# Optimization experiments

Measured on AMD Instinct MI355X. Metric: run time of the kernel, lower is better.

The kernel has to match this reference:

```python
import jax, jax.numpy as jnp
import numpy as np

N0, N1, N2, DEG = 100000, 50000, 25000, 16
IN, HID, OUT = 256, 128, 128
H1, H2 = 2, 1
E1, E2 = N1 * DEG, N2 * DEG


def setup_inputs() -> dict:
    key = jax.random.key(0)
    ks = jax.random.split(key, 16)
    x = jax.random.normal(ks[0], (N0, IN), dtype=jnp.float32)
    # neighbor-sampled bipartite edges: each dst node has DEG sampled src neighbors
    row1 = jnp.repeat(jnp.arange(N1, dtype=jnp.int32), DEG)
    col1 = jax.random.randint(ks[1], (E1,), 0, N0, dtype=jnp.int32)
    t1 = jax.random.randint(ks[2], (E1,), 0, 100, dtype=jnp.int32)
    row2 = jnp.repeat(jnp.arange(N2, dtype=jnp.int32), DEG)
    col2 = jax.random.randint(ks[3], (E2,), 0, N1, dtype=jnp.int32)
    t2 = jax.random.randint(ks[4], (E2,), 0, 100, dtype=jnp.int32)
    s_in = 1.0 / np.sqrt(IN)
    s_h = 1.0 / np.sqrt(HID)
    s_bn = 1.0 / np.sqrt(HID * H1)
    return dict(
        x=x, row1=row1, col1=col1, t1=t1, row2=row2, col2=col2, t2=t2,
        time=10, interval=20,
        Ws1=jax.random.normal(ks[5], (IN, H1 * HID), jnp.float32) * s_in,
        Wd1=jax.random.normal(ks[6], (IN, H1 * HID), jnp.float32) * s_in,
        as1=jax.random.normal(ks[7], (H1, HID), jnp.float32) * s_h,
        ad1=jax.random.normal(ks[8], (H1, HID), jnp.float32) * s_h,
        b1=jnp.zeros((H1 * HID,), jnp.float32),
        g1=jnp.ones((H1 * HID,), jnp.float32),
        beta1=jnp.zeros((H1 * HID,), jnp.float32),
        m1=jnp.zeros((H1 * HID,), jnp.float32),
        v1=jnp.ones((H1 * HID,), jnp.float32),
        Ws2=jax.random.normal(ks[9], (H1 * HID, H2 * OUT), jnp.float32) * s_bn,
        Wd2=jax.random.normal(ks[10], (H1 * HID, H2 * OUT), jnp.float32) * s_bn,
        as2=jax.random.normal(ks[11], (H2, OUT), jnp.float32) * s_h,
        ad2=jax.random.normal(ks[12], (H2, OUT), jnp.float32) * s_h,
        b2=jnp.zeros((H2 * OUT,), jnp.float32),
    )


def gat_conv(hs, hd, row, col, mask, att_s, att_d, n_dst):
    # hs: [Ns,H,C] transformed src feats, hd: [Nd,H,C]; row=dst idx, col=src idx per edge
    a_s = jnp.sum(hs * att_s, axis=-1)  # [Ns,H]
    a_d = jnp.sum(hd * att_d, axis=-1)  # [Nd,H]
    e = jax.nn.leaky_relu(a_s[col] + a_d[row], negative_slope=0.2)  # [E,H]
    e = jnp.where(mask[:, None], e, -jnp.inf)
    m = jax.ops.segment_max(e, row, num_segments=n_dst)  # [Nd,H]
    m = jnp.where(jnp.isfinite(m), m, 0.0)
    ex = jnp.where(mask[:, None], jnp.exp(e - m[row]), 0.0)
    denom = jax.ops.segment_sum(ex, row, num_segments=n_dst)
    alpha = ex / jnp.maximum(denom[row], 1e-16)  # edge softmax over incoming edges
    out = jax.ops.segment_sum(alpha[:, :, None] * hs[col], row, num_segments=n_dst)
    return out  # [Nd,H,C]


def _forward(x, Ws1, Wd1, as1, ad1, b1, g1, beta1, m1, v1,
             Ws2, Wd2, as2, ad2, b2,
             row1, col1, t1, row2, col2, t2, time, interval):
    # temporal edge masking: keep edges with timestamp in [time, time+interval)
    mask1 = (t1 >= time) & (t1 < time + interval)
    mask2 = (t2 >= time) & (t2 < time + interval)
    # ---- layer 1: GATConv(IN -> HID, heads=H1, concat=True) ----
    hs = (x @ Ws1).reshape(N0, H1, HID)
    hd = (x[:N1] @ Wd1).reshape(N1, H1, HID)
    h = gat_conv(hs, hd, row1, col1, mask1, as1, ad1, N1).reshape(N1, H1 * HID) + b1
    # BatchNorm1d (eval: running stats), then leaky_relu (slope 0.01); dropout off (eval)
    h = (h - m1) * jax.lax.rsqrt(v1 + 1e-5) * g1 + beta1
    h = jax.nn.leaky_relu(h, negative_slope=0.01)
    # ---- layer 2: GATConv(H1*HID -> OUT, heads=H2, concat=False) ----
    hs2 = (h @ Ws2).reshape(N1, H2, OUT)
    hd2 = (h[:N2] @ Wd2).reshape(N2, H2, OUT)
    out = gat_conv(hs2, hd2, row2, col2, mask2, as2, ad2, N2)
    out = jnp.mean(out, axis=1) + b2  # concat=False -> mean over heads
    return out  # [N2, OUT]


def reference(x, row1, col1, t1, row2, col2, t2, time, interval,
              Ws1, Wd1, as1, ad1, b1, g1, beta1, m1, v1,
              Ws2, Wd2, as2, ad2, b2):
    return _forward(x, Ws1, Wd1, as1, ad1, b1, g1, beta1, m1, v1,
                    Ws2, Wd2, as2, ad2, b2,
                    row1, col1, t1, row2, col2, t2, time, interval)
```

## Files before the change

kernel.cpp:

```cpp
#include <hip/hip_runtime.h>
#include <hip/hip_bf16.h>

#define N0C 100000
#define N1C 50000
#define N2C 25000

typedef _Float16 f16;
typedef _Float16 f16x2 __attribute__((ext_vector_type(2)));
typedef _Float16 f16x4 __attribute__((ext_vector_type(4)));
typedef _Float16 f16x8 __attribute__((ext_vector_type(8)));
typedef float f32x16 __attribute__((ext_vector_type(16)));

typedef const __attribute__((address_space(1))) unsigned int guint;
typedef __attribute__((address_space(3))) unsigned int luint;
__device__ __forceinline__ void gload16(const void* g, void* l) {
    __builtin_amdgcn_global_load_lds((guint*)g, (luint*)l, 16, 0, 0);
}

__device__ __forceinline__ f16x8 cvt8(float4 a, float4 b) {
    return (f16x8){(f16)a.x, (f16)a.y, (f16)a.z, (f16)a.w,
                   (f16)b.x, (f16)b.y, (f16)b.z, (f16)b.w};
}

__global__ void prep1_kernel(const float* __restrict__ Ws1, const float* __restrict__ Wd1,
                             const float* __restrict__ as1, const float* __restrict__ ad1,
                             const float* __restrict__ Ws2, const float* __restrict__ Wd2,
                             const float* __restrict__ as2, const float* __restrict__ ad2,
                             const float* __restrict__ b1, const float* __restrict__ g1,
                             const float* __restrict__ beta1, const float* __restrict__ m1,
                             const float* __restrict__ v1,
                             float* __restrict__ e1, float* __restrict__ e2,
                             float* __restrict__ bns, float* __restrict__ bnt) {
    int k = blockIdx.x, lane = threadIdx.x;
    float s0 = 0, s1 = 0, d0 = 0, d1 = 0, t0 = 0, t1 = 0;
    for (int c = lane; c < 128; c += 64) {
        s0 += Ws1[k * 256 + c] * as1[c];
        s1 += Ws1[k * 256 + 128 + c] * as1[128 + c];
        d0 += Wd1[k * 256 + c] * ad1[c];
        d1 += Wd1[k * 256 + 128 + c] * ad1[128 + c];
        t0 += Ws2[k * 128 + c] * as2[c];
        t1 += Wd2[k * 128 + c] * ad2[c];
    }
    for (int d = 1; d < 64; d <<= 1) {
        s0 += __shfl_xor(s0, d); s1 += __shfl_xor(s1, d);
        d0 += __shfl_xor(d0, d); d1 += __shfl_xor(d1, d);
        t0 += __shfl_xor(t0, d); t1 += __shfl_xor(t1, d);
    }
    if (lane == 0) {
        e1[k * 4 + 0] = s0; e1[k * 4 + 1] = s1; e1[k * 4 + 2] = d0; e1[k * 4 + 3] = d1;
        e2[k * 2 + 0] = t0; e2[k * 2 + 1] = t1;
        float sc = g1[k] * rsqrtf(v1[k] + 1e-5f);
        bns[k] = sc;
        bnt[k] = (b1[k] - m1[k]) * sc + beta1[k];
    }
}

__global__ void prep2_kernel(const float* __restrict__ Ws1, const float* __restrict__ Ws2,
                             const float* __restrict__ e1, const float* __restrict__ e2,
                             f16* __restrict__ bfl1, f16* __restrict__ bfl2) {
    int i = blockIdx.x * 256 + threadIdx.x;
    if (i < 73728) {
        int j = i & 7, lane = (i >> 3) & 63, kb = (i >> 9) & 15, nt = i >> 13;
        int c = lane & 31, hi = lane >> 5;
        int k = kb * 16 + hi * 8 + j;
        float v;
        if (nt < 8) v = Ws1[k * 256 + nt * 32 + c];
        else v = (c < 4) ? e1[k * 4 + c] : 0.f;
        bfl1[i] = (f16)v;
    } else {
        int i2 = i - 73728;
        if (i2 < 40960) {
            int j = i2 & 7, lane = (i2 >> 3) & 63, kb = (i2 >> 9) & 15, nt = i2 >> 13;
            int c = lane & 31, hi = lane >> 5;
            int k = kb * 16 + hi * 8 + j;
            float v;
            if (nt < 4) v = Ws2[k * 128 + nt * 32 + c];
            else v = (c < 2) ? e2[k * 2 + c] : 0.f;
            bfl2[i2] = (f16)v;
        }
    }
}

__global__ __launch_bounds__(512, 4) void gemm1_kernel(
    const float* __restrict__ x, const f16* __restrict__ bfl,
    f16* __restrict__ hs, float* __restrict__ as_out, float* __restrict__ ad_out) {
    __shared__ __align__(16) unsigned char smA[2][8192];
    __shared__ __align__(16) unsigned char smB[2][18432];
    const int t = threadIdx.x;
    const int wave = t >> 6, lane = t & 63;
    const int wr = wave & 3, wg = wave >> 2;
    const int col = lane & 31, hi = lane >> 5;
    const int r0 = blockIdx.x * 128;

    const int arow = t >> 2, aq = t & 3;
    const int grow_a = r0 + arow;
    const bool aval = grow_a < N0C;
    const float4* abase = (const float4*)(x + (size_t)grow_a * 256);
    const int aslot = (((arow >> 5) * 2 + (aq >> 1)) * 64 + (aq & 1) * 32 + (arow & 31)) * 16;

    float4 a0, a1;
    if (aval) { a0 = abase[aq * 2]; a1 = abase[aq * 2 + 1]; }
    else { a0 = make_float4(0.f, 0.f, 0.f, 0.f); a1 = a0; }
    for (int c = wave; c < 18; c += 8) {
        int nt = c >> 1, kbl = c & 1;
        gload16(bfl + ((size_t)(nt * 16 + kbl) * 64 + lane) * 8, smB[0] + c * 1024 + lane * 16);
    }
    *(f16x8*)(smA[0] + aslot) = cvt8(a0, a1);
    __syncthreads();

    f32x16 acc[5] = {};
    for (int ch = 0; ch < 8; ch++) {
        const int cur = ch & 1, nxt = cur ^ 1;
        const bool pre = ch < 7;
        if (pre) {
            if (aval) {
                const float4* p = abase + (ch + 1) * 8 + aq * 2;
                a0 = p[0]; a1 = p[1];
            }
            for (int c = wave; c < 18; c += 8) {
                int nt = c >> 1, kbl = c & 1;
                gload16(bfl + ((size_t)(nt * 16 + (ch + 1) * 2 + kbl) * 64 + lane) * 8,
                        smB[nxt] + c * 1024 + lane * 16);
            }
        }
#pragma unroll
        for (int kb = 0; kb < 2; kb++) {
            f16x8 af = *(const f16x8*)(smA[cur] + ((wr * 2 + kb) * 64 + lane) * 16);
            if (wg == 0) {
#pragma unroll
                for (int j = 0; j < 5; j++) {
                    f16x8 bf = *(const f16x8*)(smB[cur] + (j * 2 + kb) * 1024 + lane * 16);
                    acc[j] = __builtin_amdgcn_mfma_f32_32x32x16_f16(af, bf, acc[j], 0, 0, 0);
                }
            } else {
#pragma unroll
                for (int j = 0; j < 4; j++) {
                    f16x8 bf = *(const f16x8*)(smB[cur] + ((5 + j) * 2 + kb) * 1024 + lane * 16);
                    acc[j] = __builtin_amdgcn_mfma_f32_32x32x16_f16(af, bf, acc[j], 0, 0, 0);
                }
            }
        }
        if (pre) *(f16x8*)(smA[nxt] + aslot) = cvt8(a0, a1);
        __syncthreads();
    }

    const int rbase = r0 + wr * 32 + 4 * hi;
    if (wg == 0) {
#pragma unroll
        for (int j = 0; j < 5; j++)
#pragma unroll
            for (int r = 0; r < 16; r++) {
                int grow = rbase + (r & 3) + 8 * (r >> 2);
                if (grow < N0C) hs[(size_t)grow * 256 + j * 32 + col] = (f16)acc[j][r];
            }
    } else {
#pragma unroll
        for (int j = 0; j < 3; j++)
#pragma unroll
            for (int r = 0; r < 16; r++) {
                int grow = rbase + (r & 3) + 8 * (r >> 2);
                if (grow < N0C) hs[(size_t)grow * 256 + (5 + j) * 32 + col] = (f16)acc[j][r];
            }
#pragma unroll
        for (int r = 0; r < 16; r++) {
            int grow = rbase + (r & 3) + 8 * (r >> 2);
            float v = acc[3][r];
            if (col < 2) {
                if (grow < N0C) as_out[grow * 2 + col] = v;
            } else if (col < 4) {
                if (grow < N1C) ad_out[grow * 2 + (col - 2)] = v;
            }
        }
    }
}

__global__ __launch_bounds__(512, 4) void gemm2_kernel(
    const f16* __restrict__ h, const f16* __restrict__ bfl,
    f16* __restrict__ hs2, float* __restrict__ as_out, float* __restrict__ ad_out) {
    __shared__ __align__(16) unsigned char smA[2][8192];
    __shared__ __align__(16) unsigned char smB[2][10240];
    const int t = threadIdx.x;
    const int wave = t >> 6, lane = t & 63;
    const int wr = wave & 3, wg = wave >> 2;
    const int col = lane & 31, hi = lane >> 5;
    const int r0 = blockIdx.x * 128;

    const int wrA = wave >> 1, kbA = wave & 1;
    int arowg = r0 + wrA * 32 + col;
    if (arowg > N1C - 1) arowg = N1C - 1;
    const f16* asrc = h + (size_t)arowg * 256 + kbA * 16 + hi * 8;

    gload16(asrc, smA[0] + wave * 1024 + lane * 16);
    for (int c = wave; c < 10; c += 8) {
        int nt = c >> 1, kbl = c & 1;
        gload16(bfl + ((size_t)(nt * 16 + kbl) * 64 + lane) * 8, smB[0] + c * 1024 + lane * 16);
    }
    __syncthreads();

    f32x16 acc[3] = {};
    for (int ch = 0; ch < 8; ch++) {
        const int cur = ch & 1, nxt = cur ^ 1;
        const bool pre = ch < 7;
        if (pre) {
            gload16(asrc + (ch + 1) * 32, smA[nxt] + wave * 1024 + lane * 16);
            for (int c = wave; c < 10; c += 8) {
                int nt = c >> 1, kbl = c & 1;
                gload16(bfl + ((size_t)(nt * 16 + (ch + 1) * 2 + kbl) * 64 + lane) * 8,
                        smB[nxt] + c * 1024 + lane * 16);
            }
        }
#pragma unroll
        for (int kb = 0; kb < 2; kb++) {
            f16x8 af = *(const f16x8*)(smA[cur] + ((wr * 2 + kb) * 64 + lane) * 16);
            if (wg == 0) {
#pragma unroll
                for (int j = 0; j < 3; j++) {
                    f16x8 bf = *(const f16x8*)(smB[cur] + (j * 2 + kb) * 1024 + lane * 16);
                    acc[j] = __builtin_amdgcn_mfma_f32_32x32x16_f16(af, bf, acc[j], 0, 0, 0);
                }
            } else {
#pragma unroll
                for (int j = 0; j < 2; j++) {
                    f16x8 bf = *(const f16x8*)(smB[cur] + ((3 + j) * 2 + kb) * 1024 + lane * 16);
                    acc[j] = __builtin_amdgcn_mfma_f32_32x32x16_f16(af, bf, acc[j], 0, 0, 0);
                }
            }
        }
        __syncthreads();
    }

    const int rbase = r0 + wr * 32 + 4 * hi;
    if (wg == 0) {
#pragma unroll
        for (int j = 0; j < 3; j++)
#pragma unroll
            for (int r = 0; r < 16; r++) {
                int grow = rbase + (r & 3) + 8 * (r >> 2);
                if (grow < N1C) hs2[(size_t)grow * 128 + j * 32 + col] = (f16)acc[j][r];
            }
    } else {
#pragma unroll
        for (int r = 0; r < 16; r++) {
            int grow = rbase + (r & 3) + 8 * (r >> 2);
            if (grow < N1C) hs2[(size_t)grow * 128 + 3 * 32 + col] = (f16)acc[0][r];
        }
#pragma unroll
        for (int r = 0; r < 16; r++) {
            int grow = rbase + (r & 3) + 8 * (r >> 2);
            float v = acc[1][r];
            if (col == 0) {
                if (grow < N1C) as_out[grow] = v;
            } else if (col == 1) {
                if (grow < N2C) ad_out[grow] = v;
            }
        }
    }
}

__global__ void agg1_kernel(const int* __restrict__ col1, const int* __restrict__ t1,
                            const int* __restrict__ timep, const int* __restrict__ intervalp,
                            const float* __restrict__ a_s, const float* __restrict__ a_d,
                            const f16* __restrict__ hs,
                            const float* __restrict__ bns, const float* __restrict__ bnt,
                            f16* __restrict__ h) {
    int wid = (blockIdx.x * blockDim.x + threadIdx.x) >> 6;
    if (wid >= N1C) return;
    int lane = threadIdx.x & 63;
    int T = timep[0], I = intervalp[0];
    int j = lane & 15;
    int c = col1[wid * 16 + j];
    int tv = t1[wid * 16 + j];
    bool mk = (tv >= T) && (tv < T + I);
    float e0 = -INFINITY, e1 = -INFINITY;
    if (mk) {
        float s0 = a_s[c * 2 + 0] + a_d[wid * 2 + 0];
        float s1 = a_s[c * 2 + 1] + a_d[wid * 2 + 1];
        e0 = s0 > 0.f ? s0 : 0.2f * s0;
        e1 = s1 > 0.f ? s1 : 0.2f * s1;
    }
    float m0 = e0, m1 = e1;
#pragma unroll
    for (int d = 1; d < 16; d <<= 1) {
        m0 = fmaxf(m0, __shfl_xor(m0, d));
        m1 = fmaxf(m1, __shfl_xor(m1, d));
    }
    float ex0 = mk ? __expf(e0 - m0) : 0.f;
    float ex1 = mk ? __expf(e1 - m1) : 0.f;
    float s0 = ex0, s1 = ex1;
#pragma unroll
    for (int d = 1; d < 16; d <<= 1) {
        s0 += __shfl_xor(s0, d);
        s1 += __shfl_xor(s1, d);
    }
    float r0 = 1.f / fmaxf(s0, 1e-16f);
    float r1 = 1.f / fmaxf(s1, 1e-16f);
    unsigned long long mb = __ballot(mk) & 0xFFFFull;
    int head = lane >> 5;
    float rden = head ? r1 : r0;
    float acc0 = 0.f, acc1 = 0.f, acc2 = 0.f, acc3 = 0.f;
    while (mb) {
        int jj = __builtin_ctzll(mb);
        mb &= mb - 1;
        int cj = __shfl(c, jj);
        float w0 = __shfl(ex0, jj), w1 = __shfl(ex1, jj);
        float w = (head ? w1 : w0) * rden;
        f16x4 v = *(const f16x4*)(hs + (size_t)cj * 256 + lane * 4);
        acc0 += w * (float)v[0];
        acc1 += w * (float)v[1];
        acc2 += w * (float)v[2];
        acc3 += w * (float)v[3];
    }
    int cb = lane * 4;
    float4 sc = *(const float4*)(bns + cb);
    float4 sh = *(const float4*)(bnt + cb);
    float o0 = acc0 * sc.x + sh.x; o0 = o0 > 0.f ? o0 : 0.01f * o0;
    float o1 = acc1 * sc.y + sh.y; o1 = o1 > 0.f ? o1 : 0.01f * o1;
    float o2 = acc2 * sc.z + sh.z; o2 = o2 > 0.f ? o2 : 0.01f * o2;
    float o3 = acc3 * sc.w + sh.w; o3 = o3 > 0.f ? o3 : 0.01f * o3;
    f16x4 ov = {(f16)o0, (f16)o1, (f16)o2, (f16)o3};
    *(f16x4*)(h + (size_t)wid * 256 + cb) = ov;
}

__global__ void agg2_kernel(const int* __restrict__ col2, const int* __restrict__ t2,
                            const int* __restrict__ timep, const int* __restrict__ intervalp,
                            const float* __restrict__ a_s, const float* __restrict__ a_d,
                            const f16* __restrict__ hs2,
                            const float* __restrict__ b2, float* __restrict__ out) {
    int wid = (blockIdx.x * blockDim.x + threadIdx.x) >> 6;
    if (wid >= N2C) return;
    int lane = threadIdx.x & 63;
    int T = timep[0], I = intervalp[0];
    int j = lane & 15;
    int c = col2[wid * 16 + j];
    int tv = t2[wid * 16 + j];
    bool mk = (tv >= T) && (tv < T + I);
    float e = -INFINITY;
    if (mk) {
        float s = a_s[c] + a_d[wid];
        e = s > 0.f ? s : 0.2f * s;
    }
    float m = e;
#pragma unroll
    for (int d = 1; d < 16; d <<= 1) m = fmaxf(m, __shfl_xor(m, d));
    float ex = mk ? __expf(e - m) : 0.f;
    float s = ex;
#pragma unroll
    for (int d = 1; d < 16; d <<= 1) s += __shfl_xor(s, d);
    float r = 1.f / fmaxf(s, 1e-16f);
    unsigned long long mb = __ballot(mk) & 0xFFFFull;
    float acc0 = 0.f, acc1 = 0.f;
    while (mb) {
        int jj = __builtin_ctzll(mb);
        mb &= mb - 1;
        int cj = __shfl(c, jj);
        float w = __shfl(ex, jj) * r;
        f16x2 v = *(const f16x2*)(hs2 + (size_t)cj * 128 + lane * 2);
        acc0 += w * (float)v[0];
        acc1 += w * (float)v[1];
    }
    float2 o = make_float2(acc0 + b2[lane * 2], acc1 + b2[lane * 2 + 1]);
    *(float2*)(out + (size_t)wid * 128 + lane * 2) = o;
}

extern "C" void kernel_launch(void* const* d_in, const int* in_sizes, int n_in,
                              void* d_out, int out_size, void* d_ws, size_t ws_size,
                              hipStream_t stream) {
    const float* x = (const float*)d_in[0];
    const int* col1 = (const int*)d_in[2];
    const int* t1 = (const int*)d_in[3];
    const int* col2 = (const int*)d_in[5];
    const int* t2 = (const int*)d_in[6];
    const int* timep = (const int*)d_in[7];
    const int* intervalp = (const int*)d_in[8];
    const float* Ws1 = (const float*)d_in[9];
    const float* Wd1 = (const float*)d_in[10];
    const float* as1 = (const float*)d_in[11];
    const float* ad1 = (const float*)d_in[12];
    const float* b1 = (const float*)d_in[13];
    const float* g1 = (const float*)d_in[14];
    const float* beta1 = (const float*)d_in[15];
    const float* m1 = (const float*)d_in[16];
    const float* v1 = (const float*)d_in[17];
    const float* Ws2 = (const float*)d_in[18];
    const float* Wd2 = (const float*)d_in[19];
    const float* as2 = (const float*)d_in[20];
    const float* ad2 = (const float*)d_in[21];
    const float* b2 = (const float*)d_in[22];
    float* out = (float*)d_out;

    char* ws = (char*)d_ws;
    size_t off = 0;
    auto alloc = [&](size_t bytes) {
        size_t o = off;
        off += (bytes + 511) & ~(size_t)511;
        return o;
    };
    f16* hs = (f16*)(ws + alloc((size_t)N0C * 256 * 2));
    f16* h = (f16*)(ws + alloc((size_t)N1C * 256 * 2));
    f16* hs2 = (f16*)(ws + alloc((size_t)N1C * 128 * 2));
    float* a_s1 = (float*)(ws + alloc((size_t)N0C * 2 * 4));
    float* a_d1 = (float*)(ws + alloc((size_t)N1C * 2 * 4));
    float* a_s2 = (float*)(ws + alloc((size_t)N1C * 4));
    float* a_d2 = (float*)(ws + alloc((size_t)N2C * 4));
    f16* bfl1 = (f16*)(ws + alloc((size_t)73728 * 2));
    f16* bfl2 = (f16*)(ws + alloc((size_t)40960 * 2));
    float* e1 = (float*)(ws + alloc(1024 * 4));
    float* e2 = (float*)(ws + alloc(512 * 4));
    float* bns = (float*)(ws + alloc(256 * 4));
    float* bnt = (float*)(ws + alloc(256 * 4));

    prep1_kernel<<<256, 64, 0, stream>>>(Ws1, Wd1, as1, ad1, Ws2, Wd2, as2, ad2,
                                         b1, g1, beta1, m1, v1, e1, e2, bns, bnt);
    prep2_kernel<<<448, 256, 0, stream>>>(Ws1, Ws2, e1, e2, bfl1, bfl2);
    gemm1_kernel<<<(N0C + 127) / 128, 512, 0, stream>>>(x, bfl1, hs, a_s1, a_d1);
    agg1_kernel<<<N1C / 4, 256, 0, stream>>>(col1, t1, timep, intervalp,
                                             a_s1, a_d1, hs, bns, bnt, h);
    gemm2_kernel<<<(N1C + 127) / 128, 512, 0, stream>>>(h, bfl2, hs2, a_s2, a_d2);
    agg2_kernel<<<N2C / 4, 256, 0, stream>>>(col2, t2, timep, intervalp,
                                             a_s2, a_d2, hs2, b2, out);
}
```

Baseline: 103.7 us.

## Restructure layer-1 GEMM into 32-row tiles with split-K waves and swizzled LDS

The layer-1 projection GEMM now uses a 2D grid of 32-row tiles. Each 640-thread block loads the whole 32x256 fp32 A tile once into XOR-swizzled LDS as fp16, then gives each pair of waves one 32-column output tile with the K dimension split in half. B fragments are read straight from global memory instead of being double-buffered through LDS, and the two K halves are combined through LDS before storing. The aim is much higher parallelism and occupancy with less pipeline synchronisation, at the cost of reading the x rows twice (once per grid column) and losing row-bounds checks, which holds only because N0 is a multiple of 32.

```diff
diff --git a/kernel.cpp b/kernel.cpp
--- a/kernel.cpp
+++ b/kernel.cpp
@@ -15,11 +15,6 @@
 typedef __attribute__((address_space(3))) unsigned int luint;
 __device__ __forceinline__ void gload16(const void* g, void* l) {
     __builtin_amdgcn_global_load_lds((guint*)g, (luint*)l, 16, 0, 0);
-}
-
-__device__ __forceinline__ f16x8 cvt8(float4 a, float4 b) {
-    return (f16x8){(f16)a.x, (f16)a.y, (f16)a.z, (f16)a.w,
-                   (f16)b.x, (f16)b.y, (f16)b.z, (f16)b.w};
 }
 
 __global__ void prep1_kernel(const float* __restrict__ Ws1, const float* __restrict__ Wd1,
@@ -81,94 +76,73 @@
     }
 }
 
-__global__ __launch_bounds__(512, 4) void gemm1_kernel(
+__global__ __launch_bounds__(640, 8) void gemm1_kernel(
     const float* __restrict__ x, const f16* __restrict__ bfl,
     f16* __restrict__ hs, float* __restrict__ as_out, float* __restrict__ ad_out) {
-    __shared__ __align__(16) unsigned char smA[2][8192];
-    __shared__ __align__(16) unsigned char smB[2][18432];
+    __shared__ __align__(16) unsigned char smA[20480];
     const int t = threadIdx.x;
     const int wave = t >> 6, lane = t & 63;
-    const int wr = wave & 3, wg = wave >> 2;
+    const int ntl = wave >> 1, kh = wave & 1;
+    const int nt0 = blockIdx.x * 5 + ntl;
+    const int nt = nt0 > 8 ? 8 : nt0;
     const int col = lane & 31, hi = lane >> 5;
-    const int r0 = blockIdx.x * 128;
-
-    const int arow = t >> 2, aq = t & 3;
-    const int grow_a = r0 + arow;
-    const bool aval = grow_a < N0C;
-    const float4* abase = (const float4*)(x + (size_t)grow_a * 256);
-    const int aslot = (((arow >> 5) * 2 + (aq >> 1)) * 64 + (aq & 1) * 32 + (arow & 31)) * 16;
-
-    float4 a0, a1;
-    if (aval) { a0 = abase[aq * 2]; a1 = abase[aq * 2 + 1]; }
-    else { a0 = make_float4(0.f, 0.f, 0.f, 0.f); a1 = a0; }
-    for (int c = wave; c < 18; c += 8) {
-        int nt = c >> 1, kbl = c & 1;
-        gload16(bfl + ((size_t)(nt * 16 + kbl) * 64 + lane) * 8, smB[0] + c * 1024 + lane * 16);
-    }
-    *(f16x8*)(smA[0] + aslot) = cvt8(a0, a1);
+    const int r0 = blockIdx.y * 32;
+
+    if (t < 512) {
+        int r = t >> 4, s = t & 15;
+        const float4* src = (const float4*)(x + (size_t)(r0 + r) * 256) + s;
+#pragma unroll
+        for (int p = 0; p < 4; p++) {
+            float4 v = src[16 * p];
+            int q = s + 16 * p;
+            int kb = q >> 2, hp = (q >> 1) & 1, hf = q & 1;
+            f16x4 h4 = {(f16)v.x, (f16)v.y, (f16)v.z, (f16)v.w};
+            int byt = (((kb * 64 + hp * 32 + r) * 16) ^ ((kb & 7) << 4)) + hf * 8;
+            *(f16x4*)(smA + byt) = h4;
+        }
+    }
     __syncthreads();
 
-    f32x16 acc[5] = {};
-    for (int ch = 0; ch < 8; ch++) {
-        const int cur = ch & 1, nxt = cur ^ 1;
-        const bool pre = ch < 7;
-        if (pre) {
-            if (aval) {
-                const float4* p = abase + (ch + 1) * 8 + aq * 2;
-                a0 = p[0]; a1 = p[1];
-            }
-            for (int c = wave; c < 18; c += 8) {
-                int nt = c >> 1, kbl = c & 1;
-                gload16(bfl + ((size_t)(nt * 16 + (ch + 1) * 2 + kbl) * 64 + lane) * 8,
-                        smB[nxt] + c * 1024 + lane * 16);
-            }
-        }
-#pragma unroll
-        for (int kb = 0; kb < 2; kb++) {
-            f16x8 af = *(const f16x8*)(smA[cur] + ((wr * 2 + kb) * 64 + lane) * 16);
-            if (wg == 0) {
-#pragma unroll
-                for (int j = 0; j < 5; j++) {
-                    f16x8 bf = *(const f16x8*)(smB[cur] + (j * 2 + kb) * 1024 + lane * 16);
-                    acc[j] = __builtin_amdgcn_mfma_f32_32x32x16_f16(af, bf, acc[j], 0, 0, 0);
+    f32x16 acc = {};
+#pragma unroll
+    for (int g = 0; g < 2; g++) {
+        f16x8 b[4];
+#pragma unroll
+        for (int i = 0; i < 4; i++)
+            b[i] = *(const f16x8*)(bfl + ((size_t)(nt * 16 + kh * 8 + g * 4 + i) * 64 + lane) * 8);
+#pragma unroll
+        for (int i = 0; i < 4; i++) {
+            int kb = kh * 8 + g * 4 + i;
+            f16x8 af = *(const f16x8*)(smA + (((kb * 64 + hi * 32 + col) * 16) ^ ((kb & 7) << 4)));
+            acc = __builtin_amdgcn_mfma_f32_32x32x16_f16(af, b[i], acc, 0, 0, 0);
+        }
+    }
+    __syncthreads();
+
+    float* rb = (float*)smA;
+    if (kh == 1) {
+#pragma unroll
+        for (int r = 0; r < 16; r++) rb[(r * 5 + ntl) * 64 + lane] = acc[r];
+    }
+    __syncthreads();
+    if (kh == 0 && nt0 <= 8) {
+        if (nt0 < 8) {
+#pragma unroll
+            for (int r = 0; r < 16; r++) {
+                int grow = r0 + (r & 3) + 8 * (r >> 2) + 4 * hi;
+                hs[(size_t)grow * 256 + nt0 * 32 + col] =
+                    (f16)(acc[r] + rb[(r * 5 + ntl) * 64 + lane]);
+            }
+        } else {
+#pragma unroll
+            for (int r = 0; r < 16; r++) {
+                int grow = r0 + (r & 3) + 8 * (r >> 2) + 4 * hi;
+                float v = acc[r] + rb[(r * 5 + ntl) * 64 + lane];
+                if (col < 2) {
+                    as_out[grow * 2 + col] = v;
+                } else if (col < 4) {
+                    if (grow < N1C) ad_out[grow * 2 + (col - 2)] = v;
                 }
-            } else {
-#pragma unroll
-                for (int j = 0; j < 4; j++) {
-                    f16x8 bf = *(const f16x8*)(smB[cur] + ((5 + j) * 2 + kb) * 1024 + lane * 16);
-                    acc[j] = __builtin_amdgcn_mfma_f32_32x32x16_f16(af, bf, acc[j], 0, 0, 0);
-                }
-            }
-        }
-        if (pre) *(f16x8*)(smA[nxt] + aslot) = cvt8(a0, a1);
-        __syncthreads();
-    }
-
-    const int rbase = r0 + wr * 32 + 4 * hi;
-    if (wg == 0) {
-#pragma unroll
-        for (int j = 0; j < 5; j++)
-#pragma unroll
-            for (int r = 0; r < 16; r++) {
-                int grow = rbase + (r & 3) + 8 * (r >> 2);
-                if (grow < N0C) hs[(size_t)grow * 256 + j * 32 + col] = (f16)acc[j][r];
-            }
-    } else {
-#pragma unroll
-        for (int j = 0; j < 3; j++)
-#pragma unroll
-            for (int r = 0; r < 16; r++) {
-                int grow = rbase + (r & 3) + 8 * (r >> 2);
-                if (grow < N0C) hs[(size_t)grow * 256 + (5 + j) * 32 + col] = (f16)acc[j][r];
-            }
-#pragma unroll
-        for (int r = 0; r < 16; r++) {
-            int grow = rbase + (r & 3) + 8 * (r >> 2);
-            float v = acc[3][r];
-            if (col < 2) {
-                if (grow < N0C) as_out[grow * 2 + col] = v;
-            } else if (col < 4) {
-                if (grow < N1C) ad_out[grow * 2 + (col - 2)] = v;
             }
         }
     }
@@ -412,7 +386,7 @@
     prep1_kernel<<<256, 64, 0, stream>>>(Ws1, Wd1, as1, ad1, Ws2, Wd2, as2, ad2,
                                          b1, g1, beta1, m1, v1, e1, e2, bns, bnt);
     prep2_kernel<<<448, 256, 0, stream>>>(Ws1, Ws2, e1, e2, bfl1, bfl2);
-    gemm1_kernel<<<(N0C + 127) / 128, 512, 0, stream>>>(x, bfl1, hs, a_s1, a_d1);
+    gemm1_kernel<<<dim3(2, 3125), 640, 0, stream>>>(x, bfl1, hs, a_s1, a_d1);
     agg1_kernel<<<N1C / 4, 256, 0, stream>>>(col1, t1, timep, intervalp,
                                              a_s1, a_d1, hs, bns, bnt, h);
     gemm2_kernel<<<(N1C + 127) / 128, 512, 0, stream>>>(h, bfl2, hs2, a_s2, a_d2);
```

Measured after the change: 112.1 us. 1.08x slower.

## Stream fp32 A tiles directly into LDS via async loads with XOR swizzle

Applied to the files above, without the earlier changes.

The GEMM1 A operand (x in fp32) is now fetched with global_load_lds directly into a doubled-size LDS buffer using an XOR-swizzled layout, instead of loading through registers, converting to fp16 and storing to LDS. The fp32 to fp16 conversion moves to after the LDS read in each MFMA k-step. The aim is to drop register staging and the synchronous store, letting A loads overlap like the B loads already do. In exchange it doubles A's LDS footprint, which may reduce occupancy, and each wave repeats the conversions. Out-of-range rows are clamped to the last row instead of being zero-filled.

```diff
diff --git a/kernel.cpp b/kernel.cpp
--- a/kernel.cpp
+++ b/kernel.cpp
@@ -15,11 +15,6 @@
 typedef __attribute__((address_space(3))) unsigned int luint;
 __device__ __forceinline__ void gload16(const void* g, void* l) {
     __builtin_amdgcn_global_load_lds((guint*)g, (luint*)l, 16, 0, 0);
-}
-
-__device__ __forceinline__ f16x8 cvt8(float4 a, float4 b) {
-    return (f16x8){(f16)a.x, (f16)a.y, (f16)a.z, (f16)a.w,
-                   (f16)b.x, (f16)b.y, (f16)b.z, (f16)b.w};
 }
 
 __global__ void prep1_kernel(const float* __restrict__ Ws1, const float* __restrict__ Wd1,
@@ -84,7 +79,7 @@
 __global__ __launch_bounds__(512, 4) void gemm1_kernel(
     const float* __restrict__ x, const f16* __restrict__ bfl,
     f16* __restrict__ hs, float* __restrict__ as_out, float* __restrict__ ad_out) {
-    __shared__ __align__(16) unsigned char smA[2][8192];
+    __shared__ __align__(16) unsigned char smA[2][16384];
     __shared__ __align__(16) unsigned char smB[2][18432];
     const int t = threadIdx.x;
     const int wave = t >> 6, lane = t & 63;
@@ -92,31 +87,37 @@
     const int col = lane & 31, hi = lane >> 5;
     const int r0 = blockIdx.x * 128;
 
-    const int arow = t >> 2, aq = t & 3;
-    const int grow_a = r0 + arow;
-    const bool aval = grow_a < N0C;
-    const float4* abase = (const float4*)(x + (size_t)grow_a * 256);
-    const int aslot = (((arow >> 5) * 2 + (aq >> 1)) * 64 + (aq & 1) * 32 + (arow & 31)) * 16;
-
-    float4 a0, a1;
-    if (aval) { a0 = abase[aq * 2]; a1 = abase[aq * 2 + 1]; }
-    else { a0 = make_float4(0.f, 0.f, 0.f, 0.f); a1 = a0; }
+    int arow[2], ag[2];
+#pragma unroll
+    for (int p = 0; p < 2; p++) {
+        int s = (wave * 2 + p) * 64 + lane;
+        int row = s >> 3;
+        ag[p] = (s & 7) ^ (row & 7);
+        int rc = r0 + row;
+        arow[p] = rc > N0C - 1 ? N0C - 1 : rc;
+    }
+
+#pragma unroll
+    for (int p = 0; p < 2; p++)
+        gload16(x + (size_t)arow[p] * 256 + ag[p] * 4,
+                smA[0] + ((wave * 2 + p) * 64 + lane) * 16);
     for (int c = wave; c < 18; c += 8) {
         int nt = c >> 1, kbl = c & 1;
         gload16(bfl + ((size_t)(nt * 16 + kbl) * 64 + lane) * 8, smB[0] + c * 1024 + lane * 16);
     }
-    *(f16x8*)(smA[0] + aslot) = cvt8(a0, a1);
     __syncthreads();
 
     f32x16 acc[5] = {};
+    const int myrow = wr * 32 + col;
+    const int m7 = myrow & 7;
     for (int ch = 0; ch < 8; ch++) {
         const int cur = ch & 1, nxt = cur ^ 1;
         const bool pre = ch < 7;
         if (pre) {
-            if (aval) {
-                const float4* p = abase + (ch + 1) * 8 + aq * 2;
-                a0 = p[0]; a1 = p[1];
-            }
+#pragma unroll
+            for (int p = 0; p < 2; p++)
+                gload16(x + (size_t)arow[p] * 256 + (ch + 1) * 32 + ag[p] * 4,
+                        smA[nxt] + ((wave * 2 + p) * 64 + lane) * 16);
             for (int c = wave; c < 18; c += 8) {
                 int nt = c >> 1, kbl = c & 1;
                 gload16(bfl + ((size_t)(nt * 16 + (ch + 1) * 2 + kbl) * 64 + lane) * 8,
@@ -125,7 +126,11 @@
         }
 #pragma unroll
         for (int kb = 0; kb < 2; kb++) {
-            f16x8 af = *(const f16x8*)(smA[cur] + ((wr * 2 + kb) * 64 + lane) * 16);
+            int ob = kb * 4 + hi * 2;
+            float4 fa = *(const float4*)(smA[cur] + (myrow * 8 + (ob ^ m7)) * 16);
+            float4 fb = *(const float4*)(smA[cur] + (myrow * 8 + ((ob + 1) ^ m7)) * 16);
+            f16x8 af = {(f16)fa.x, (f16)fa.y, (f16)fa.z, (f16)fa.w,
+                        (f16)fb.x, (f16)fb.y, (f16)fb.z, (f16)fb.w};
             if (wg == 0) {
 #pragma unroll
                 for (int j = 0; j < 5; j++) {
@@ -140,7 +145,6 @@
                 }
             }
         }
-        if (pre) *(f16x8*)(smA[nxt] + aslot) = cvt8(a0, a1);
         __syncthreads();
     }
 
```

New measurement: 102.7 us. Within noise of the previous version (-1.0%).
